# Performance work log

Measured on AMD Instinct MI355X. Metric: run time of the kernel, lower is better.

## Reference

```python
import jax, jax.numpy as jnp
import numpy as np

D_MODEL = 2048
N_HEADS = 16
HEAD_DIM = D_MODEL // N_HEADS


def setup_inputs() -> dict:
    key = jax.random.key(0)
    ks = jax.random.split(key, 5)
    scale = 1.0 / np.sqrt(D_MODEL)
    x = jax.random.normal(ks[0], (2, 2048, D_MODEL), dtype=jnp.float32)
    W_qkv = jax.random.normal(ks[1], (D_MODEL, 3 * D_MODEL), dtype=jnp.float32) * scale
    b_qkv = jnp.zeros((3 * D_MODEL,), dtype=jnp.float32)
    W_out = jax.random.normal(ks[2], (D_MODEL, D_MODEL), dtype=jnp.float32) * scale
    b_out = jnp.zeros((D_MODEL,), dtype=jnp.float32)
    return {"x": x, "W_qkv": W_qkv, "b_qkv": b_qkv, "W_out": W_out, "b_out": b_out}


def reference(x, W_qkv, b_qkv, W_out, b_out):
    bsz, seq_len, _ = x.shape
    # QKV projection: (b, s, 3*d) -> (3, b, h, s, hd)
    qkv = x @ W_qkv + b_qkv
    qkv = qkv.reshape(bsz, seq_len, 3, N_HEADS, HEAD_DIM)
    qkv = jnp.transpose(qkv, (2, 0, 3, 1, 4))
    q, k, v = qkv[0], qkv[1], qkv[2]
    # scaled dot-product scores: (b, h, s, s)
    scores = jnp.einsum("bhqd,bhkd->bhqk", q, k) / np.sqrt(HEAD_DIM).astype(np.float32)
    causal = jnp.tril(jnp.ones((seq_len, seq_len), dtype=bool))
    scores = jnp.where(causal[None, None], scores, -jnp.inf)
    attn = jax.nn.softmax(scores, axis=-1)
    # attention output: (b, h, s, hd) -> (b, s, d)
    out = jnp.einsum("bhqk,bhkd->bhqd", attn, v)
    out = jnp.transpose(out, (0, 2, 1, 3)).reshape(bsz, seq_len, D_MODEL)
    y = out @ W_out + b_out
    return y
```

## Files before the change

### kernel.cpp

```cpp
#include <hip/hip_runtime.h>
#include <stdint.h>
#include <stddef.h>


typedef __attribute__((ext_vector_type(8))) short bf16x8;
typedef __attribute__((ext_vector_type(4))) float f32x4;

#define SOFT_SCALE 0.12751743075419806f

__device__ __forceinline__ short f2bf(float f) {
  union { float f; unsigned u; } v; v.f = f;
  unsigned u = v.u + 0x7fffu + ((v.u >> 16) & 1u);
  return (short)(u >> 16);
}

__device__ __forceinline__ void gload_lds16(const void* g, const void* l) {
  __builtin_amdgcn_global_load_lds(
      (__attribute__((address_space(1))) void*)(uintptr_t)g,
      (__attribute__((address_space(3))) void*)(uintptr_t)l,
      16, 0, 0);
}

__global__ __launch_bounds__(256) void cast_f32_bf16(
    const float* __restrict__ in, short* __restrict__ out, int n8) {
  int i = blockIdx.x * 256 + threadIdx.x;
  if (i >= n8) return;
  float4 a = ((const float4*)in)[i * 2];
  float4 b = ((const float4*)in)[i * 2 + 1];
  bf16x8 o;
  o[0] = f2bf(a.x); o[1] = f2bf(a.y); o[2] = f2bf(a.z); o[3] = f2bf(a.w);
  o[4] = f2bf(b.x); o[5] = f2bf(b.y); o[6] = f2bf(b.z); o[7] = f2bf(b.w);
  ((bf16x8*)out)[i] = o;
}

__global__ __launch_bounds__(256) void transpose_cast_w(
    const float* __restrict__ W, short* __restrict__ WT, int K, int N) {
  __shared__ short t[32][33];
  int k0 = blockIdx.x * 32, n0 = blockIdx.y * 32;
  int r = threadIdx.x >> 3;
  int c = (threadIdx.x & 7) * 4;
  float4 v = *(const float4*)(W + (size_t)(k0 + r) * N + n0 + c);
  t[r][c + 0] = f2bf(v.x); t[r][c + 1] = f2bf(v.y);
  t[r][c + 2] = f2bf(v.z); t[r][c + 3] = f2bf(v.w);
  __syncthreads();
  short4 o;
  o.x = t[c + 0][r]; o.y = t[c + 1][r]; o.z = t[c + 2][r]; o.w = t[c + 3][r];
  *(short4*)(WT + (size_t)(n0 + r) * K + k0 + c) = o;
}

template <int BF16OUT, int VTRANS, int QSCALE>
__global__ __launch_bounds__(256) void gemm_bt(
    const short* __restrict__ A, const short* __restrict__ BT,
    void* __restrict__ Cv, const float* __restrict__ bias,
    short* __restrict__ vTout, int M, int N, int K) {
  __shared__ __align__(16) short SH[17408];
  const int tid = threadIdx.x;
  const int wave = tid >> 6, lane = tid & 63;
  const int quad = lane >> 4, l16 = lane & 15;
  const int wmg = (wave >> 1) * 4;
  const int wng = (wave & 1) * 4;
  const int m0 = blockIdx.x * 128, n0 = blockIdx.y * 128;
  const int srow = lane >> 2;
  const int scol = (lane & 3) * 8;

  const short* aptr[2];
  const short* bptr[2];
#pragma unroll
  for (int it = 0; it < 2; ++it) {
    int c = wave * 2 + it;
    aptr[it] = A + (size_t)(m0 + c * 16 + srow) * K + scol;
    bptr[it] = BT + (size_t)(n0 + c * 16 + srow) * K + scol;
  }

  f32x4 acc[4][4] = {};

  auto stage = [&](int buf) {
#pragma unroll
    for (int it = 0; it < 2; ++it) {
      int c = wave * 2 + it;
      gload_lds16(aptr[it], (const char*)SH + buf * 8192 + c * 1024);
      gload_lds16(bptr[it], (const char*)SH + 16384 + buf * 8192 + c * 1024);
    }
#pragma unroll
    for (int it = 0; it < 2; ++it) { aptr[it] += 32; bptr[it] += 32; }
  };

  stage(0);
  const int nIter = K >> 5;
  for (int i = 0; i < nIter; ++i) {
    const int buf = i & 1;
    __syncthreads();
    if (i + 1 < nIter) stage(1 - buf);
    const short* As = SH + buf * 4096;
    const short* Bs = SH + 8192 + buf * 4096;
    bf16x8 af[4], bfg[4];
#pragma unroll
    for (int t = 0; t < 4; ++t)
      af[t] = *(const bf16x8*)(As + (wmg + t) * 512 + l16 * 32 + quad * 8);
#pragma unroll
    for (int t = 0; t < 4; ++t)
      bfg[t] = *(const bf16x8*)(Bs + (wng + t) * 512 + l16 * 32 + quad * 8);
#pragma unroll
    for (int tm = 0; tm < 4; ++tm)
#pragma unroll
      for (int tn = 0; tn < 4; ++tn)
        acc[tm][tn] = __builtin_amdgcn_mfma_f32_16x16x32_bf16(
            af[tm], bfg[tn], acc[tm][tn], 0, 0, 0);
  }

  if (VTRANS && n0 >= 4096) {
    __syncthreads();
#pragma unroll
    for (int tn = 0; tn < 4; ++tn) {
      int hd = (wng + tn) * 16 + l16;
      float bv = bias[n0 + hd];
#pragma unroll
      for (int tm = 0; tm < 4; ++tm) {
        int sl = (wmg + tm) * 16 + quad * 4;
#pragma unroll
        for (int r = 0; r < 4; ++r)
          SH[hd * 136 + sl + r] = f2bf(acc[tm][tn][r] + bv);
      }
    }
    __syncthreads();
    const int bb = m0 >> 11, s0 = m0 & 2047, hd0 = n0 - 4096;
#pragma unroll
    for (int pass = 0; pass < 8; ++pass) {
      int row = pass * 16 + (tid >> 4);
      int c16 = (tid & 15) * 8;
      bf16x8 v = *(const bf16x8*)(SH + row * 136 + c16);
      *(bf16x8*)(vTout + ((size_t)(bb * 2048 + hd0 + row)) * 2048 + s0 + c16) =
          v;
    }
    return;
  }

#pragma unroll
  for (int tn = 0; tn < 4; ++tn) {
    int n = n0 + (wng + tn) * 16 + l16;
    float bv = bias[n];
#pragma unroll
    for (int tm = 0; tm < 4; ++tm) {
      int mb = m0 + (wmg + tm) * 16 + quad * 4;
#pragma unroll
      for (int r = 0; r < 4; ++r) {
        float v = acc[tm][tn][r] + bv;
        if (QSCALE && n < 2048) v *= SOFT_SCALE;
        if (BF16OUT)
          ((short*)Cv)[(size_t)(mb + r) * N + n] = f2bf(v);
        else
          ((float*)Cv)[(size_t)(mb + r) * N + n] = v;
      }
    }
  }
}

__global__ __launch_bounds__(512, 4) void attn_kernel(
    const short* __restrict__ qkv, const short* __restrict__ vT,
    short* __restrict__ obuf) {
  __shared__ __align__(16) short Ks[2 * 8192];
  __shared__ __align__(16) short Vs[2 * 8192];
  __shared__ __align__(16) short Ps[8192];
  const int tid = threadIdx.x;
  const int wave = tid >> 6, lane = tid & 63;
  const int quad = lane >> 4, l16 = lane & 15;
  const int bh = blockIdx.y, b = bh >> 4, h = bh & 15;
  const int px = blockIdx.x;
  const int p = (blockIdx.y & 16) ? (15 - px) : px;
  const int q0 = p * 128;
  const int nkt = 2 * (p + 1);

  const short* qbase = qkv + (size_t)b * 2048 * 6144 + h * 128;
  const short* kbase = qkv + (size_t)b * 2048 * 6144 + 2048 + h * 128;
  const short* vtbase = vT + (size_t)bh * 128 * 2048;
  short* obase = obuf + (size_t)b * 2048 * 2048 + h * 128;

  const int srow = lane >> 2;
  const int scol = (lane & 3) * 8;

  bf16x8 ones;
#pragma unroll
  for (int j = 0; j < 8; ++j) ones[j] = (short)0x3F80;

  bf16x8 qf[4];
#pragma unroll
  for (int kk = 0; kk < 4; ++kk)
    qf[kk] = *(const bf16x8*)(
        qbase + (size_t)(q0 + wave * 16 + l16) * 6144 + kk * 32 + quad * 8);

  f32x4 acco[8] = {};
  f32x4 accl = {};

  auto stage = [&](int buf, int kt) {
    const int k0 = kt * 64;
#pragma unroll
    for (int it = 0; it < 2; ++it) {
      int c = wave * 2 + it;
      gload_lds16(
          kbase + (size_t)(k0 + (c & 3) * 16 + srow) * 6144 + (c >> 2) * 32 +
              scol,
          (const char*)Ks + buf * 16384 + c * 1024);
    }
#pragma unroll
    for (int it = 0; it < 2; ++it) {
      int c = wave * 2 + it;
      gload_lds16(
          vtbase + (size_t)((c & 7) * 16 + srow) * 2048 + k0 + (c >> 3) * 32 +
              scol,
          (const char*)Vs + buf * 16384 + c * 1024);
    }
  };

  stage(0, 0);

  for (int kt = 0; kt < nkt; ++kt) {
    const int buf = kt & 1;
    __syncthreads();
    if (kt + 1 < nkt) stage(1 - buf, kt + 1);
    const short* KsB = Ks + buf * 8192;
    const short* VsB = Vs + buf * 8192;

    f32x4 accs[4] = {};
#pragma unroll
    for (int kk = 0; kk < 4; ++kk) {
      bf16x8 bfg[4];
#pragma unroll
      for (int tn = 0; tn < 4; ++tn)
        bfg[tn] = *(const bf16x8*)(KsB + (kk * 4 + tn) * 512 + l16 * 32 +
                                   quad * 8);
#pragma unroll
      for (int tn = 0; tn < 4; ++tn)
        accs[tn] = __builtin_amdgcn_mfma_f32_16x16x32_bf16(
            qf[kk], bfg[tn], accs[tn], 0, 0, 0);
    }

    if (kt >= nkt - 2) {
      const int k0 = kt * 64;
#pragma unroll
      for (int tn = 0; tn < 4; ++tn)
#pragma unroll
        for (int r = 0; r < 4; ++r) {
          int grow = q0 + wave * 16 + quad * 4 + r;
          int gcol = k0 + tn * 16 + l16;
          if (gcol > grow) accs[tn][r] = -1e30f;
        }
    }
#pragma unroll
    for (int tn = 0; tn < 4; ++tn)
#pragma unroll
      for (int r = 0; r < 4; ++r) accs[tn][r] = exp2f(accs[tn][r]);

#pragma unroll
    for (int r = 0; r < 4; ++r)
#pragma unroll
      for (int tn = 0; tn < 4; ++tn)
        Ps[wave * 1024 + (tn >> 1) * 512 + (quad * 4 + r) * 32 +
           (tn & 1) * 16 + l16] = f2bf(accs[tn][r]);

#pragma unroll
    for (int kk2 = 0; kk2 < 2; ++kk2) {
      bf16x8 av = *(const bf16x8*)(Ps + wave * 1024 + kk2 * 512 + l16 * 32 +
                                   quad * 8);
      accl = __builtin_amdgcn_mfma_f32_16x16x32_bf16(av, ones, accl, 0, 0, 0);
      bf16x8 bfg[8];
#pragma unroll
      for (int tn = 0; tn < 8; ++tn)
        bfg[tn] = *(const bf16x8*)(VsB + (kk2 * 8 + tn) * 512 + l16 * 32 +
                                   quad * 8);
#pragma unroll
      for (int tn = 0; tn < 8; ++tn)
        acco[tn] = __builtin_amdgcn_mfma_f32_16x16x32_bf16(
            av, bfg[tn], acco[tn], 0, 0, 0);
    }
  }

  float inv[4];
#pragma unroll
  for (int r = 0; r < 4; ++r) inv[r] = 1.f / accl[r];
#pragma unroll
  for (int r = 0; r < 4; ++r) {
    int row = q0 + wave * 16 + quad * 4 + r;
#pragma unroll
    for (int tn = 0; tn < 8; ++tn)
      obase[(size_t)row * 2048 + tn * 16 + l16] = f2bf(acco[tn][r] * inv[r]);
  }
}

extern "C" void kernel_launch(void* const* d_in, const int* in_sizes, int n_in,
                              void* d_out, int out_size, void* d_ws,
                              size_t ws_size, hipStream_t stream) {
  (void)in_sizes; (void)n_in; (void)out_size; (void)ws_size;
  const float* x    = (const float*)d_in[0];
  const float* Wqkv = (const float*)d_in[1];
  const float* bqkv = (const float*)d_in[2];
  const float* Wout = (const float*)d_in[3];
  const float* bout = (const float*)d_in[4];
  float* out = (float*)d_out;

  char* ws = (char*)d_ws;
  short* xb    = (short*)(ws);
  short* wqkvT = (short*)(ws + 16777216);
  short* woutT = (short*)(ws + 41943040);
  short* qkv   = (short*)(ws + 50331648);
  short* vTb   = (short*)(ws + 100663296);
  short* obuf  = (short*)(ws + 117440512);

  cast_f32_bf16<<<4096, 256, 0, stream>>>(x, xb, 1048576);
  transpose_cast_w<<<dim3(64, 192), 256, 0, stream>>>(Wqkv, wqkvT, 2048, 6144);
  transpose_cast_w<<<dim3(64, 64), 256, 0, stream>>>(Wout, woutT, 2048, 2048);

  gemm_bt<1, 1, 1><<<dim3(32, 48), 256, 0, stream>>>(
      xb, wqkvT, (void*)qkv, bqkv, vTb, 4096, 6144, 2048);

  attn_kernel<<<dim3(16, 32), 512, 0, stream>>>(qkv, vTb, obuf);

  gemm_bt<0, 0, 0><<<dim3(32, 16), 256, 0, stream>>>(
      obuf, woutT, (void*)out, bout, nullptr, 4096, 2048, 2048);
}
```

Measured before the change: 360.8 us.

## Replace GEMM with 256x128-tile, 3-stage pipelined, swizzled-LDS kernel

The projection GEMMs now use 256x128 output tiles with 512 threads, a 64-wide K step and a three-buffer global-to-LDS pipeline driven by explicit vmcnt waits and barriers. The LDS layout is XOR-swizzled to avoid bank conflicts, and the block index is remapped to group neighbouring tiles for L2 reuse. MFMA phases are split so B loads and staging overlap compute, with s_setprio raised during MFMA. This targets the large QKV and output GEMMs that surround attention, at the cost of higher LDS use (about 144KB per block) and lower occupancy.

```diff
diff --git a/kernel.cpp b/kernel.cpp
--- a/kernel.cpp
+++ b/kernel.cpp
@@ -49,102 +49,164 @@
 }
 
 template <int BF16OUT, int VTRANS, int QSCALE>
-__global__ __launch_bounds__(256) void gemm_bt(
+__global__ __launch_bounds__(512, 2) void gemm256(
     const short* __restrict__ A, const short* __restrict__ BT,
     void* __restrict__ Cv, const float* __restrict__ bias,
     short* __restrict__ vTout, int M, int N, int K) {
-  __shared__ __align__(16) short SH[17408];
+  (void)M;
+  __shared__ __align__(16) short SH[73728];
   const int tid = threadIdx.x;
   const int wave = tid >> 6, lane = tid & 63;
   const int quad = lane >> 4, l16 = lane & 15;
-  const int wmg = (wave >> 1) * 4;
-  const int wng = (wave & 1) * 4;
-  const int m0 = blockIdx.x * 128, n0 = blockIdx.y * 128;
-  const int srow = lane >> 2;
-  const int scol = (lane & 3) * 8;
-
-  const short* aptr[2];
-  const short* bptr[2];
-#pragma unroll
-  for (int it = 0; it < 2; ++it) {
-    int c = wave * 2 + it;
-    aptr[it] = A + (size_t)(m0 + c * 16 + srow) * K + scol;
-    bptr[it] = BT + (size_t)(n0 + c * 16 + srow) * K + scol;
-  }
+  const int wm = wave >> 1, wn = wave & 1;
+  const int kx = (l16 & 7) << 3;
+
+  const int gx = gridDim.x;
+  int bid = blockIdx.y * gx + blockIdx.x;
+  const int nwg = gx * gridDim.y;
+  bid = (bid & 7) * (nwg >> 3) + (bid >> 3);
+  const int m0 = (bid % gx) * 256, n0 = (bid / gx) * 128;
+
+  const int rsub = lane >> 3;
+  const int csub = ((lane & 7) ^ rsub) << 3;
+  const short* aS[4];
+  const short* bS[2];
+#pragma unroll
+  for (int i = 0; i < 4; ++i)
+    aS[i] = A + (size_t)(m0 + (wave * 4 + i) * 8 + rsub) * K + csub;
+#pragma unroll
+  for (int i = 0; i < 2; ++i)
+    bS[i] = BT + (size_t)(n0 + (wave * 2 + i) * 8 + rsub) * K + csub;
+
+  auto stageA = [&](int st, int sb) {
+#pragma unroll
+    for (int i = 0; i < 4; ++i)
+      gload_lds16(aS[i] + st * 64,
+                  (const char*)SH + sb * 49152 + (wave * 4 + i) * 1024);
+  };
+  auto stageB = [&](int st, int sb) {
+#pragma unroll
+    for (int i = 0; i < 2; ++i)
+      gload_lds16(bS[i] + st * 64,
+                  (const char*)SH + sb * 49152 + 32768 + (wave * 2 + i) * 1024);
+  };
+
+  stageA(0, 0); stageB(0, 0);
+  stageA(1, 1); stageB(1, 1);
 
   f32x4 acc[4][4] = {};
-
-  auto stage = [&](int buf) {
-#pragma unroll
-    for (int it = 0; it < 2; ++it) {
-      int c = wave * 2 + it;
-      gload_lds16(aptr[it], (const char*)SH + buf * 8192 + c * 1024);
-      gload_lds16(bptr[it], (const char*)SH + 16384 + buf * 8192 + c * 1024);
-    }
-#pragma unroll
-    for (int it = 0; it < 2; ++it) { aptr[it] += 32; bptr[it] += 32; }
-  };
-
-  stage(0);
-  const int nIter = K >> 5;
-  for (int i = 0; i < nIter; ++i) {
-    const int buf = i & 1;
-    __syncthreads();
-    if (i + 1 < nIter) stage(1 - buf);
-    const short* As = SH + buf * 4096;
-    const short* Bs = SH + 8192 + buf * 4096;
-    bf16x8 af[4], bfg[4];
-#pragma unroll
-    for (int t = 0; t < 4; ++t)
-      af[t] = *(const bf16x8*)(As + (wmg + t) * 512 + l16 * 32 + quad * 8);
-#pragma unroll
-    for (int t = 0; t < 4; ++t)
-      bfg[t] = *(const bf16x8*)(Bs + (wng + t) * 512 + l16 * 32 + quad * 8);
-#pragma unroll
-    for (int tm = 0; tm < 4; ++tm)
-#pragma unroll
-      for (int tn = 0; tn < 4; ++tn)
-        acc[tm][tn] = __builtin_amdgcn_mfma_f32_16x16x32_bf16(
-            af[tm], bfg[tn], acc[tm][tn], 0, 0, 0);
+  const int nT = K >> 6;
+  int buf = 0, sb = 2;
+  for (int t = 0; t < nT; ++t) {
+    const int st = (t + 2 < nT) ? (t + 2) : (nT - 1);
+    const short* As = (const short*)((const char*)SH + buf * 49152);
+    const short* Bs = As + 16384;
+
+    asm volatile("s_waitcnt vmcnt(6)" ::: "memory");
+    __builtin_amdgcn_s_barrier();
+
+    bf16x8 af[4][2], bf[2][2];
+#pragma unroll
+    for (int f = 0; f < 4; ++f) {
+      const int row = wm * 64 + f * 16 + l16;
+#pragma unroll
+      for (int kk = 0; kk < 2; ++kk)
+        af[f][kk] = *(const bf16x8*)(As + row * 64 +
+                                     (((kk << 5) | (quad << 3)) ^ kx));
+    }
+#pragma unroll
+    for (int u = 0; u < 2; ++u) {
+      const int row = wn * 64 + u * 16 + l16;
+#pragma unroll
+      for (int kk = 0; kk < 2; ++kk)
+        bf[u][kk] = *(const bf16x8*)(Bs + row * 64 +
+                                     (((kk << 5) | (quad << 3)) ^ kx));
+    }
+    stageA(st, sb);
+    __builtin_amdgcn_s_barrier();
+    asm volatile("s_waitcnt lgkmcnt(0)" ::: "memory");
+    __builtin_amdgcn_sched_barrier(0);
+    __builtin_amdgcn_s_setprio(1);
+#pragma unroll
+    for (int f = 0; f < 4; ++f)
+#pragma unroll
+      for (int u = 0; u < 2; ++u)
+#pragma unroll
+        for (int kk = 0; kk < 2; ++kk)
+          acc[f][u] = __builtin_amdgcn_mfma_f32_16x16x32_bf16(
+              af[f][kk], bf[u][kk], acc[f][u], 0, 0, 0);
+    __builtin_amdgcn_s_setprio(0);
+    __builtin_amdgcn_s_barrier();
+
+#pragma unroll
+    for (int u = 0; u < 2; ++u) {
+      const int row = wn * 64 + 32 + u * 16 + l16;
+#pragma unroll
+      for (int kk = 0; kk < 2; ++kk)
+        bf[u][kk] = *(const bf16x8*)(Bs + row * 64 +
+                                     (((kk << 5) | (quad << 3)) ^ kx));
+    }
+    stageB(st, sb);
+    __builtin_amdgcn_s_barrier();
+    asm volatile("s_waitcnt lgkmcnt(0)" ::: "memory");
+    __builtin_amdgcn_sched_barrier(0);
+    __builtin_amdgcn_s_setprio(1);
+#pragma unroll
+    for (int f = 0; f < 4; ++f)
+#pragma unroll
+      for (int u = 0; u < 2; ++u)
+#pragma unroll
+        for (int kk = 0; kk < 2; ++kk)
+          acc[f][2 + u] = __builtin_amdgcn_mfma_f32_16x16x32_bf16(
+              af[f][kk], bf[u][kk], acc[f][2 + u], 0, 0, 0);
+    __builtin_amdgcn_s_setprio(0);
+
+    buf = (buf == 2) ? 0 : buf + 1;
+    sb = (sb == 2) ? 0 : sb + 1;
   }
 
   if (VTRANS && n0 >= 4096) {
-    __syncthreads();
-#pragma unroll
-    for (int tn = 0; tn < 4; ++tn) {
-      int hd = (wng + tn) * 16 + l16;
-      float bv = bias[n0 + hd];
-#pragma unroll
-      for (int tm = 0; tm < 4; ++tm) {
-        int sl = (wmg + tm) * 16 + quad * 4;
-#pragma unroll
-        for (int r = 0; r < 4; ++r)
-          SH[hd * 136 + sl + r] = f2bf(acc[tm][tn][r] + bv);
+    asm volatile("s_waitcnt vmcnt(0)" ::: "memory");
+    __builtin_amdgcn_s_barrier();
+    short* T = (short*)SH;
+#pragma unroll
+    for (int j = 0; j < 4; ++j) {
+      const int nl = wn * 64 + j * 16 + l16;
+      const float bv = bias[n0 + nl];
+#pragma unroll
+      for (int f = 0; f < 4; ++f) {
+        const int ml = wm * 64 + f * 16 + quad * 4;
+        short4 o;
+        o.x = f2bf(acc[f][j][0] + bv);
+        o.y = f2bf(acc[f][j][1] + bv);
+        o.z = f2bf(acc[f][j][2] + bv);
+        o.w = f2bf(acc[f][j][3] + bv);
+        *(short4*)(T + nl * 264 + ml) = o;
       }
     }
-    __syncthreads();
-    const int bb = m0 >> 11, s0 = m0 & 2047, hd0 = n0 - 4096;
+    __builtin_amdgcn_s_barrier();
+    const int b = m0 >> 11, s0 = m0 & 2047, h = (n0 - 4096) >> 7;
 #pragma unroll
     for (int pass = 0; pass < 8; ++pass) {
-      int row = pass * 16 + (tid >> 4);
-      int c16 = (tid & 15) * 8;
-      bf16x8 v = *(const bf16x8*)(SH + row * 136 + c16);
-      *(bf16x8*)(vTout + ((size_t)(bb * 2048 + hd0 + row)) * 2048 + s0 + c16) =
-          v;
+      const int row = pass * 16 + (tid >> 5);
+      const int c = (tid & 31) * 8;
+      bf16x8 v = *(const bf16x8*)(T + row * 264 + c);
+      *(bf16x8*)(vTout + ((size_t)((b * 16 + h) * 128 + row)) * 2048 + s0 +
+                 c) = v;
     }
     return;
   }
 
 #pragma unroll
-  for (int tn = 0; tn < 4; ++tn) {
-    int n = n0 + (wng + tn) * 16 + l16;
-    float bv = bias[n];
-#pragma unroll
-    for (int tm = 0; tm < 4; ++tm) {
-      int mb = m0 + (wmg + tm) * 16 + quad * 4;
+  for (int j = 0; j < 4; ++j) {
+    const int n = n0 + wn * 64 + j * 16 + l16;
+    const float bv = bias[n];
+#pragma unroll
+    for (int f = 0; f < 4; ++f) {
+      const int mb = m0 + wm * 64 + f * 16 + quad * 4;
 #pragma unroll
       for (int r = 0; r < 4; ++r) {
-        float v = acc[tm][tn][r] + bv;
+        float v = acc[f][j][r] + bv;
         if (QSCALE && n < 2048) v *= SOFT_SCALE;
         if (BF16OUT)
           ((short*)Cv)[(size_t)(mb + r) * N + n] = f2bf(v);
@@ -309,11 +371,11 @@
   transpose_cast_w<<<dim3(64, 192), 256, 0, stream>>>(Wqkv, wqkvT, 2048, 6144);
   transpose_cast_w<<<dim3(64, 64), 256, 0, stream>>>(Wout, woutT, 2048, 2048);
 
-  gemm_bt<1, 1, 1><<<dim3(32, 48), 256, 0, stream>>>(
+  gemm256<1, 1, 1><<<dim3(16, 48), 512, 0, stream>>>(
       xb, wqkvT, (void*)qkv, bqkv, vTb, 4096, 6144, 2048);
 
   attn_kernel<<<dim3(16, 32), 512, 0, stream>>>(qkv, vTb, obuf);
 
-  gemm_bt<0, 0, 0><<<dim3(32, 16), 256, 0, stream>>>(
+  gemm256<0, 0, 0><<<dim3(16, 16), 512, 0, stream>>>(
       obuf, woutT, (void*)out, bout, nullptr, 4096, 2048, 2048);
 }
```

Measured after the change: 363.6 us. No clear change (+0.8%).
